# Optimization experiments

Measured on AMD Instinct MI355X. Metric: run time of the kernel, lower is better.

The kernel has to match this reference:

```python
import jax, jax.numpy as jnp
import numpy as np

C = 256
HEADS = 8
HD = C // HEADS
EPS = 1e-5


def _layernorm(x, g, b):
    mu = jnp.mean(x, axis=-1, keepdims=True)
    var = jnp.var(x, axis=-1, keepdims=True)
    return (x - mu) * jax.lax.rsqrt(var + EPS) * g + b


def setup_inputs() -> dict:
    key = jax.random.key(0)
    ks = jax.random.split(key, 16)
    s = 0.02
    return {
        "x": jax.random.normal(ks[0], (1, C, 64, 64), jnp.float32),
        "bn_gamma": 1.0 + s * jax.random.normal(ks[1], (C,), jnp.float32),
        "bn_beta": s * jax.random.normal(ks[2], (C,), jnp.float32),
        "bn_mean": s * jax.random.normal(ks[3], (C,), jnp.float32),
        "bn_var": jnp.ones((C,), jnp.float32),
        "w_in": s * jax.random.normal(ks[4], (C, C), jnp.float32),
        "b_in": jnp.zeros((C,), jnp.float32),
        "ln1_g": jnp.ones((C,), jnp.float32),
        "ln1_b": jnp.zeros((C,), jnp.float32),
        "w_qkv": s * jax.random.normal(ks[5], (3 * C, C), jnp.float32),
        "b_qkv": jnp.zeros((3 * C,), jnp.float32),
        "w_ap": s * jax.random.normal(ks[6], (C, C), jnp.float32),
        "b_ap": jnp.zeros((C,), jnp.float32),
        "ln2_g": jnp.ones((C,), jnp.float32),
        "ln2_b": jnp.zeros((C,), jnp.float32),
        "w_ff1": s * jax.random.normal(ks[7], (4 * C, C), jnp.float32),
        "b_ff1": jnp.zeros((4 * C,), jnp.float32),
        "w_ff2": s * jax.random.normal(ks[8], (C, 4 * C), jnp.float32),
        "b_ff2": jnp.zeros((C,), jnp.float32),
        "w_out": s * jax.random.normal(ks[9], (C, C), jnp.float32),
        "b_out": jnp.zeros((C,), jnp.float32),
    }


def reference(x, bn_gamma, bn_beta, bn_mean, bn_var, w_in, b_in,
              ln1_g, ln1_b, w_qkv, b_qkv, w_ap, b_ap,
              ln2_g, ln2_b, w_ff1, b_ff1, w_ff2, b_ff2, w_out, b_out):
    b, c, h, w = x.shape
    t = h * w
    x_in = x
    # BatchNorm2d (eval mode: running stats)
    xn = (x - bn_mean[None, :, None, None]) * jax.lax.rsqrt(bn_var + EPS)[None, :, None, None]
    xn = xn * bn_gamma[None, :, None, None] + bn_beta[None, :, None, None]
    # proj_in 1x1 conv -> tokens [b, t, c]
    tok = xn.reshape(b, c, t).transpose(0, 2, 1)
    tok = tok @ w_in.T + b_in
    # transformer block (depth=1)
    y = _layernorm(tok, ln1_g, ln1_b)  # norm1
    qkv = y @ w_qkv.T + b_qkv  # [b, t, 3c], channel split (3, H, hd)
    qkv = qkv.reshape(b, t, 3, HEADS, HD)
    q = qkv[:, :, 0].transpose(0, 2, 1, 3)  # [b, H, t, hd]
    k = qkv[:, :, 1].transpose(0, 2, 1, 3)
    v = qkv[:, :, 2].transpose(0, 2, 1, 3)
    scale = HD ** (-0.5)
    attn = jax.nn.softmax(jnp.einsum('bhqd,bhkd->bhqk', q, k) * scale, axis=-1)
    o = jnp.einsum('bhqk,bhkd->bhqd', attn, v)  # [b, H, t, hd]
    o = o.transpose(0, 2, 1, 3).reshape(b, t, c)  # channels ordered (H, hd)
    o = o @ w_ap.T + b_ap  # attn proj 1x1
    attn_out = o + y  # VanillaAttention residual adds its (normed) input
    tok = tok + attn_out
    # FFN
    z = _layernorm(tok, ln2_g, ln2_b)
    z = jax.nn.gelu(z @ w_ff1.T + b_ff1, approximate=False)
    tok = tok + (z @ w_ff2.T + b_ff2)
    # back to image, proj_out 1x1, outer residual
    x4 = tok.transpose(0, 2, 1).reshape(b, c, h, w)
    out = jnp.einsum('oc,bchw->bohw', w_out, x4) + b_out[None, :, None, None]
    return out + x_in
```

## Files before the change

kernel.cpp:

```cpp
#include <hip/hip_runtime.h>
#include <math.h>

#define T_TOK 4096
#define C_DIM 256
#define EPSF  1e-5f
#define SC_QL (0.17677669529663687f * 1.4426950408889634f)

typedef short  bf16x8  __attribute__((ext_vector_type(8)));
typedef float  f32x4   __attribute__((ext_vector_type(4)));
typedef ushort ushort8 __attribute__((ext_vector_type(8)));

__device__ __forceinline__ short f2bf(float f) {
    unsigned u = __builtin_bit_cast(unsigned, f);
    unsigned r = (u + 0x7FFFu + ((u >> 16) & 1u)) >> 16;
    return (short)r;
}
__device__ __forceinline__ float bf2f(ushort u) {
    return __builtin_bit_cast(float, ((unsigned)u) << 16);
}
__device__ __forceinline__ unsigned pk_bf16(float a, float b) {
    const unsigned ua = __builtin_bit_cast(unsigned, a) + 0x8000u;
    const unsigned ub = __builtin_bit_cast(unsigned, b) + 0x8000u;
    return __builtin_amdgcn_perm(ub, ua, 0x07060302u);
}
template <int CTRL>
__device__ __forceinline__ float dppf(float x) {
    return __builtin_bit_cast(float,
        __builtin_amdgcn_mov_dpp(__builtin_bit_cast(int, x), CTRL, 0xF, 0xF, true));
}
__device__ __forceinline__ float rowsum16(float x) {
    x += dppf<0xB1>(x);
    x += dppf<0x4E>(x);
    x += dppf<0x141>(x);
    x += dppf<0x140>(x);
    return x;
}
#define MFMA16(a, b, c) __builtin_amdgcn_mfma_f32_16x16x32_bf16(a, b, c, 0, 0, 0)

__global__ __launch_bounds__(256) void prep_kernel(
    const float* __restrict__ w_in, const float* __restrict__ w_qkv,
    const float* __restrict__ w_ap, const float* __restrict__ w_ff1,
    const float* __restrict__ w_ff2, const float* __restrict__ w_out,
    const float* __restrict__ b_qkv, const float* __restrict__ b_ff1,
    const float* __restrict__ ln1_g, const float* __restrict__ ln1_b,
    const float* __restrict__ ln2_g, const float* __restrict__ ln2_b,
    ushort* __restrict__ wbuf, float* __restrict__ u_all, float* __restrict__ d_all,
    const float* __restrict__ x, const float* __restrict__ gamma,
    const float* __restrict__ beta, const float* __restrict__ mean,
    const float* __restrict__ var, ushort* __restrict__ tin)
{
    __shared__ float tile[32][33];
    if (blockIdx.x < 896) {
        const int gid = blockIdx.x * 256 + threadIdx.x;
        const int e0 = gid * 4;
        const float* src; int off;
        float4 sc = {1.f, 1.f, 1.f, 1.f};
        if (e0 < 65536)       { src = w_in;  off = e0; }
        else if (e0 < 262144) {
            src = w_qkv; off = e0 - 65536;
            const int k = off & 255;
            sc = *(const float4*)(ln1_g + k);
            if (off < 65536) { sc.x *= SC_QL; sc.y *= SC_QL; sc.z *= SC_QL; sc.w *= SC_QL; }
        }
        else if (e0 < 327680) { src = w_ap;  off = e0 - 262144; }
        else if (e0 < 589824) {
            src = w_ff1; off = e0 - 327680;
            sc = *(const float4*)(ln2_g + (off & 255));
        }
        else if (e0 < 851968) { src = w_ff2; off = e0 - 589824; }
        else                  { src = w_out; off = e0 - 851968; }
        const float4 v = *(const float4*)(src + off);
        ushort4 o;
        o.x = (ushort)f2bf(v.x * sc.x); o.y = (ushort)f2bf(v.y * sc.y);
        o.z = (ushort)f2bf(v.z * sc.z); o.w = (ushort)f2bf(v.w * sc.w);
        *(ushort4*)(wbuf + e0) = o;
    } else if (blockIdx.x < 1920) {
        const int bidx = blockIdx.x - 896;
        const int t0 = (bidx & 127) * 32, c0 = (bidx >> 7) * 32;
        const int tx = threadIdx.x & 31, ty = threadIdx.x >> 5;
#pragma unroll
        for (int i = 0; i < 32; i += 8) {
            const int c = c0 + ty + i;
            const float a = rsqrtf(var[c] + EPSF) * gamma[c];
            const float d = beta[c] - mean[c] * a;
            tile[ty + i][tx] = x[c * T_TOK + t0 + tx] * a + d;
        }
        __syncthreads();
#pragma unroll
        for (int i = 0; i < 32; i += 8) {
            const int t = t0 + ty + i;
            tin[t * C_DIM + c0 + tx] = (ushort)f2bf(tile[tx][ty + i]);
        }
    } else {
        const int row = (blockIdx.x - 1920) * 4 + (threadIdx.x >> 6);
        const int lane = threadIdx.x & 63;
        const float* W; const float* gv; const float* bv; float bias; float qs = 1.f;
        if (row < 768) {
            W = w_qkv + (size_t)row * 256; gv = ln1_g; bv = ln1_b; bias = b_qkv[row];
            if (row < 256) qs = SC_QL;
        } else {
            const int r2 = row - 768;
            W = w_ff1 + (size_t)r2 * 256; gv = ln2_g; bv = ln2_b; bias = b_ff1[r2];
        }
        const float4 w4 = *(const float4*)(W + lane * 4);
        const float4 g4 = *(const float4*)(gv + lane * 4);
        const float4 b4 = *(const float4*)(bv + lane * 4);
        float su = w4.x * g4.x + w4.y * g4.y + w4.z * g4.z + w4.w * g4.w;
        float sd = w4.x * b4.x + w4.y * b4.y + w4.z * b4.z + w4.w * b4.w;
#pragma unroll
        for (int off = 32; off > 0; off >>= 1) {
            su += __shfl_xor(su, off);
            sd += __shfl_xor(sd, off);
        }
        if (lane == 0) {
            u_all[row] = qs * su;
            d_all[row] = qs * (sd + bias);
        }
    }
}

__global__ __launch_bounds__(1024) void fused_pre(
    const ushort* __restrict__ tin, const ushort* __restrict__ wb_in,
    const float* __restrict__ b_in, const ushort* __restrict__ wb_qkv,
    const float* __restrict__ u_all, const float* __restrict__ d_all,
    float* __restrict__ tok0, float* __restrict__ lnstats,
    ushort* __restrict__ qkvb)
{
    __shared__ ushort Atile[16 * 264];
    __shared__ ushort Vt[16 * 264];
    __shared__ float  red[16][16][2];
    const int t0 = blockIdx.x * 16;
    const int tid = threadIdx.x, wv = tid >> 6, lane = tid & 63;
    const int c = lane & 15, g = lane >> 4;

    bf16x8 w1[8];
#pragma unroll
    for (int kc = 0; kc < 8; ++kc)
        w1[kc] = *(const bf16x8*)(wb_in + (size_t)(wv * 16 + c) * 256 + kc * 32 + g * 8);

    {
        const int r = tid >> 6, c0 = (tid & 63) * 4;
        *(ushort4*)&Atile[r * 264 + c0] = *(const ushort4*)(tin + (size_t)(t0 + r) * 256 + c0);
    }
    __syncthreads();

    f32x4 acc1 = {};
#pragma unroll
    for (int kc = 0; kc < 8; ++kc) {
        const bf16x8 af = *(const bf16x8*)&Atile[c * 264 + kc * 32 + g * 8];
        acc1 = MFMA16(af, w1[kc], acc1);
    }
    const int colp = wv * 16 + c;
    float vs[4];
    {
        const float bb = b_in[colp];
        float s1[4], s2[4];
#pragma unroll
        for (int rr = 0; rr < 4; ++rr) {
            const float v = acc1[rr] + bb;
            vs[rr] = v; s1[rr] = v; s2[rr] = v * v;
            tok0[(size_t)(t0 + 4 * g + rr) * 256 + colp] = v;
            Vt[(4 * g + rr) * 264 + colp] = (ushort)f2bf(v);
        }
#pragma unroll
        for (int rr = 0; rr < 4; ++rr) { s1[rr] = rowsum16(s1[rr]); s2[rr] = rowsum16(s2[rr]); }
        if (c == 0) {
#pragma unroll
            for (int rr = 0; rr < 4; ++rr) {
                red[wv][4 * g + rr][0] = s1[rr];
                red[wv][4 * g + rr][1] = s2[rr];
            }
        }
    }
    __syncthreads();

    if (tid < 32) {
        const int row = tid >> 1, j = tid & 1;
        float s = 0.f;
#pragma unroll
        for (int w = 0; w < 16; ++w) s += red[w][row][j];
        red[0][row][j] = s;
    }

    f32x4 acc2[3] = {};
#pragma unroll
    for (int kc = 0; kc < 8; ++kc) {
        const bf16x8 af = *(const bf16x8*)&Vt[c * 264 + kc * 32 + g * 8];
#pragma unroll
        for (int nf = 0; nf < 3; ++nf) {
            const bf16x8 bfv = *(const bf16x8*)(wb_qkv +
                (size_t)(wv * 48 + nf * 16 + c) * 256 + kc * 32 + g * 8);
            acc2[nf] = MFMA16(af, bfv, acc2[nf]);
        }
    }
    __syncthreads();

    float mu[4], rs[4];
#pragma unroll
    for (int rr = 0; rr < 4; ++rr) {
        const int row = 4 * g + rr;
        mu[rr] = red[0][row][0] * (1.0f / 256.0f);
        const float var = red[0][row][1] * (1.0f / 256.0f) - mu[rr] * mu[rr];
        rs[rr] = rsqrtf(var + EPSF);
    }
    if (wv == 0 && c == 0) {
#pragma unroll
        for (int rr = 0; rr < 4; ++rr) {
            lnstats[(size_t)(t0 + 4 * g + rr) * 2 + 0] = mu[rr];
            lnstats[(size_t)(t0 + 4 * g + rr) * 2 + 1] = rs[rr];
        }
    }
#pragma unroll
    for (int nf = 0; nf < 3; ++nf) {
        const int col = wv * 48 + nf * 16 + c;
        const float u = u_all[col], d = d_all[col];
#pragma unroll
        for (int rr = 0; rr < 4; ++rr) {
            const float q = rs[rr] * (acc2[nf][rr] - mu[rr] * u) + d;
            qkvb[(size_t)(t0 + 4 * g + rr) * 768 + col] = (ushort)f2bf(q);
        }
    }
}

#define KS   40
#define VTS  72
#define PS_W 34

__global__ __launch_bounds__(256) void attn_mfma(
    const ushort* __restrict__ qkv, ushort* __restrict__ opart,
    float* __restrict__ lpart)
{
    const int h    = blockIdx.y;
    const int q0   = blockIdx.x << 6;
    const int half = blockIdx.z;
    const int tid  = threadIdx.x;
    const int wv   = tid >> 6, lane = tid & 63;
    const int c    = lane & 15, g = lane >> 4;

    __shared__ ushort Ks[2][64 * KS];
    __shared__ ushort Vt[2][32 * VTS];
    __shared__ float  Ps[4][16 * PS_W];

    const bf16x8 qf = *(const bf16x8*)(qkv + (size_t)(q0 + wv * 16 + c) * 768 + h * 32 + g * 8);

    bf16x8 ones;
#pragma unroll
    for (int i = 0; i < 8; ++i) ones[i] = (short)0x3F80;

    f32x4 oacc0 = {0.f, 0.f, 0.f, 0.f};
    f32x4 oacc1 = {0.f, 0.f, 0.f, 0.f};
    f32x4 oaccl = {0.f, 0.f, 0.f, 0.f};

    const int kr = tid >> 2, kc = (tid & 3) * 8;
    const int vp = tid & 31, vd = (tid >> 5) * 4;
    const ushort* kbase = qkv + 256 + h * 32;
    const ushort* vbase = qkv + 512 + h * 32;

    const int kt0 = half * 16, kt1 = kt0 + 16;
    ushort8 kpre  = *(const ushort8*)(kbase + ((size_t)kt0 * 64 + kr) * 768 + kc);
    ushort4 vpre0 = *(const ushort4*)(vbase + ((size_t)kt0 * 64 + 2 * vp) * 768 + vd);
    ushort4 vpre1 = *(const ushort4*)(vbase + ((size_t)kt0 * 64 + 2 * vp + 1) * 768 + vd);

    int p = 0;
    for (int kt = kt0; kt < kt1; ++kt) {
        *(ushort8*)&Ks[p][kr * KS + kc] = kpre;
        {
            unsigned* vtp = (unsigned*)&Vt[p][0];
            vtp[(vd + 0) * (VTS / 2) + vp] = (unsigned)vpre0.x | ((unsigned)vpre1.x << 16);
            vtp[(vd + 1) * (VTS / 2) + vp] = (unsigned)vpre0.y | ((unsigned)vpre1.y << 16);
            vtp[(vd + 2) * (VTS / 2) + vp] = (unsigned)vpre0.z | ((unsigned)vpre1.z << 16);
            vtp[(vd + 3) * (VTS / 2) + vp] = (unsigned)vpre0.w | ((unsigned)vpre1.w << 16);
        }
        __syncthreads();
        if (kt + 1 < kt1) {
            const size_t t0 = (size_t)(kt + 1) * 64;
            kpre  = *(const ushort8*)(kbase + (t0 + kr) * 768 + kc);
            vpre0 = *(const ushort4*)(vbase + (t0 + 2 * vp) * 768 + vd);
            vpre1 = *(const ushort4*)(vbase + (t0 + 2 * vp + 1) * 768 + vd);
        }

        const ushort* ks = &Ks[p][0];
        const ushort* vt = &Vt[p][0];
        const f32x4 zz = {0.f, 0.f, 0.f, 0.f};
        const bf16x8 k0 = *(const bf16x8*)&ks[(0 * 16 + c) * KS + g * 8];
        const bf16x8 k1 = *(const bf16x8*)&ks[(1 * 16 + c) * KS + g * 8];
        const bf16x8 k2 = *(const bf16x8*)&ks[(2 * 16 + c) * KS + g * 8];
        const bf16x8 k3 = *(const bf16x8*)&ks[(3 * 16 + c) * KS + g * 8];
        const f32x4 s0 = MFMA16(k0, qf, zz);
        const f32x4 s1 = MFMA16(k1, qf, zz);
        const f32x4 s2 = MFMA16(k2, qf, zz);
        const f32x4 s3 = MFMA16(k3, qf, zz);

        float* prow = &Ps[wv][c * PS_W];
        {
            const float e00 = __builtin_amdgcn_exp2f(s0[0]), e01 = __builtin_amdgcn_exp2f(s0[1]);
            const float e02 = __builtin_amdgcn_exp2f(s0[2]), e03 = __builtin_amdgcn_exp2f(s0[3]);
            const float e10 = __builtin_amdgcn_exp2f(s1[0]), e11 = __builtin_amdgcn_exp2f(s1[1]);
            const float e12 = __builtin_amdgcn_exp2f(s1[2]), e13 = __builtin_amdgcn_exp2f(s1[3]);
            const float e20 = __builtin_amdgcn_exp2f(s2[0]), e21 = __builtin_amdgcn_exp2f(s2[1]);
            const float e22 = __builtin_amdgcn_exp2f(s2[2]), e23 = __builtin_amdgcn_exp2f(s2[3]);
            const float e30 = __builtin_amdgcn_exp2f(s3[0]), e31 = __builtin_amdgcn_exp2f(s3[1]);
            const float e32 = __builtin_amdgcn_exp2f(s3[2]), e33 = __builtin_amdgcn_exp2f(s3[3]);
            prow[0 * 8 + 2 * g + 0] = __builtin_bit_cast(float, pk_bf16(e00, e01));
            prow[0 * 8 + 2 * g + 1] = __builtin_bit_cast(float, pk_bf16(e02, e03));
            prow[1 * 8 + 2 * g + 0] = __builtin_bit_cast(float, pk_bf16(e10, e11));
            prow[1 * 8 + 2 * g + 1] = __builtin_bit_cast(float, pk_bf16(e12, e13));
            prow[2 * 8 + 2 * g + 0] = __builtin_bit_cast(float, pk_bf16(e20, e21));
            prow[2 * 8 + 2 * g + 1] = __builtin_bit_cast(float, pk_bf16(e22, e23));
            prow[3 * 8 + 2 * g + 0] = __builtin_bit_cast(float, pk_bf16(e30, e31));
            prow[3 * 8 + 2 * g + 1] = __builtin_bit_cast(float, pk_bf16(e32, e33));
        }
#pragma unroll
        for (int ch = 0; ch < 2; ++ch) {
            const float2 pA = *(const float2*)&prow[ch * 16 + 4 * g];
            const float2 pB = *(const float2*)&prow[ch * 16 + 4 * g + 2];
            unsigned pw[4];
            pw[0] = __builtin_bit_cast(unsigned, pA.x);
            pw[1] = __builtin_bit_cast(unsigned, pA.y);
            pw[2] = __builtin_bit_cast(unsigned, pB.x);
            pw[3] = __builtin_bit_cast(unsigned, pB.y);
            const bf16x8 pf = *(const bf16x8*)pw;
            const bf16x8 v0 = *(const bf16x8*)&vt[(c)      * VTS + ch * 32 + g * 8];
            const bf16x8 v1 = *(const bf16x8*)&vt[(16 + c) * VTS + ch * 32 + g * 8];
            oacc0 = MFMA16(pf, v0, oacc0);
            oacc1 = MFMA16(pf, v1, oacc1);
            oaccl = MFMA16(pf, ones, oaccl);
        }
        p ^= 1;
        __syncthreads();
    }

    {
        ushort* op = opart + (size_t)half * (1u << 20) + (size_t)(q0 + wv * 16) * 256 + h * 32;
#pragma unroll
        for (int rr = 0; rr < 4; ++rr) {
            op[(4 * g + rr) * 256 + c]      = (ushort)f2bf(oacc0[rr]);
            op[(4 * g + rr) * 256 + 16 + c] = (ushort)f2bf(oacc1[rr]);
        }
        if (c == 0) {
#pragma unroll
            for (int rr = 0; rr < 4; ++rr)
                lpart[(size_t)(q0 + wv * 16 + 4 * g + rr) * 32 + half * 8 + h] = oaccl[rr];
        }
    }
}

__global__ __launch_bounds__(1024) void fused_mid(
    const ushort* __restrict__ opart, const float* __restrict__ lpart,
    const ushort* __restrict__ wb_ap, const float* __restrict__ b_ap,
    const float* __restrict__ tok0, const float* __restrict__ lnstats,
    const float* __restrict__ ln1_g, const float* __restrict__ ln1_b,
    const ushort* __restrict__ wb_ff1, const float* __restrict__ u_all,
    const float* __restrict__ d_all, float* __restrict__ tok1,
    ushort* __restrict__ zbuf)
{
    __shared__ ushort Otile[16 * 264];
    __shared__ ushort Vt[16 * 264];
    __shared__ float  red[16][16][2];
    const int t0 = blockIdx.x * 16;
    const int tid = threadIdx.x, wv = tid >> 6, lane = tid & 63;
    const int c = lane & 15, g = lane >> 4;

    bf16x8 w1[8];
#pragma unroll
    for (int kc = 0; kc < 8; ++kc)
        w1[kc] = *(const bf16x8*)(wb_ap + (size_t)(wv * 16 + c) * 256 + kc * 32 + g * 8);

    {
        const int r = tid >> 6, c0 = (tid & 63) * 4;
        const int h = (tid & 63) >> 3;
        const float* lp = lpart + (size_t)(t0 + r) * 32;
        const float inv = 1.0f / (lp[h] + lp[8 + h] + lp[16 + h] + lp[24 + h]);
        const size_t base = (size_t)(t0 + r) * 256 + c0;
        const ushort4 a0 = *(const ushort4*)(opart + base);
        const ushort4 a1 = *(const ushort4*)(opart + (1u << 20) + base);
        const ushort4 a2 = *(const ushort4*)(opart + (2u << 20) + base);
        const ushort4 a3 = *(const ushort4*)(opart + (3u << 20) + base);
        unsigned w[2];
        w[0] = pk_bf16((bf2f(a0.x) + bf2f(a1.x) + bf2f(a2.x) + bf2f(a3.x)) * inv,
                       (bf2f(a0.y) + bf2f(a1.y) + bf2f(a2.y) + bf2f(a3.y)) * inv);
        w[1] = pk_bf16((bf2f(a0.z) + bf2f(a1.z) + bf2f(a2.z) + bf2f(a3.z)) * inv,
                       (bf2f(a0.w) + bf2f(a1.w) + bf2f(a2.w) + bf2f(a3.w)) * inv);
        *(ushort4*)&Otile[r * 264 + c0] = *(ushort4*)w;
    }
    __syncthreads();

    f32x4 acc1 = {};
#pragma unroll
    for (int kc = 0; kc < 8; ++kc) {
        const bf16x8 af = *(const bf16x8*)&Otile[c * 264 + kc * 32 + g * 8];
        acc1 = MFMA16(af, w1[kc], acc1);
    }
    const int colp = wv * 16 + c;
    {
        const float bb = b_ap[colp];
        const float g1 = ln1_g[colp], b1 = ln1_b[colp];
        float s1[4], s2[4];
#pragma unroll
        for (int rr = 0; rr < 4; ++rr) {
            const int row = t0 + 4 * g + rr;
            const size_t idx = (size_t)row * 256 + colp;
            const float t0v = tok0[idx];
            const float mu1 = lnstats[(size_t)row * 2 + 0];
            const float rs1 = lnstats[(size_t)row * 2 + 1];
            const float y = (t0v - mu1) * rs1 * g1 + b1;
            const float v = acc1[rr] + bb + y + t0v;
            s1[rr] = v; s2[rr] = v * v;
            tok1[idx] = v;
            Vt[(4 * g + rr) * 264 + colp] = (ushort)f2bf(v);
        }
#pragma unroll
        for (int rr = 0; rr < 4; ++rr) { s1[rr] = rowsum16(s1[rr]); s2[rr] = rowsum16(s2[rr]); }
        if (c == 0) {
#pragma unroll
            for (int rr = 0; rr < 4; ++rr) {
                red[wv][4 * g + rr][0] = s1[rr];
                red[wv][4 * g + rr][1] = s2[rr];
            }
        }
    }
    __syncthreads();

    if (tid < 32) {
        const int row = tid >> 1, j = tid & 1;
        float s = 0.f;
#pragma unroll
        for (int w = 0; w < 16; ++w) s += red[w][row][j];
        red[0][row][j] = s;
    }

    f32x4 acc2[4] = {};
#pragma unroll
    for (int kc = 0; kc < 8; ++kc) {
        const bf16x8 af = *(const bf16x8*)&Vt[c * 264 + kc * 32 + g * 8];
#pragma unroll
        for (int nf = 0; nf < 4; ++nf) {
            const bf16x8 bfv = *(const bf16x8*)(wb_ff1 +
                (size_t)(wv * 64 + nf * 16 + c) * 256 + kc * 32 + g * 8);
            acc2[nf] = MFMA16(af, bfv, acc2[nf]);
        }
    }
    __syncthreads();

    float mu[4], rs[4];
#pragma unroll
    for (int rr = 0; rr < 4; ++rr) {
        const int row = 4 * g + rr;
        mu[rr] = red[0][row][0] * (1.0f / 256.0f);
        const float var = red[0][row][1] * (1.0f / 256.0f) - mu[rr] * mu[rr];
        rs[rr] = rsqrtf(var + EPSF);
    }
#pragma unroll
    for (int nf = 0; nf < 4; ++nf) {
        const int col = wv * 64 + nf * 16 + c;
        const float u = u_all[768 + col], d = d_all[768 + col];
#pragma unroll
        for (int rr = 0; rr < 4; ++rr) {
            float v = rs[rr] * (acc2[nf][rr] - mu[rr] * u) + d;
            v = 0.5f * v * (1.0f + erff(v * 0.70710678118654752f));
            zbuf[(size_t)(t0 + 4 * g + rr) * 1024 + col] = (ushort)f2bf(v);
        }
    }
}

__global__ __launch_bounds__(1024) void fused_post(
    const ushort* __restrict__ zbuf, const ushort* __restrict__ wb_ff2,
    const float* __restrict__ b_ff2, const float* __restrict__ tok1,
    const ushort* __restrict__ wb_out, const float* __restrict__ b_out,
    const float* __restrict__ x, float* __restrict__ out)
{
    __shared__ ushort Ztile[16 * 1032];
    __shared__ ushort T2tile[16 * 264];
    const int t0 = blockIdx.x * 16;
    const int tid = threadIdx.x, wv = tid >> 6, lane = tid & 63;
    const int c = lane & 15, g = lane >> 4;

    bf16x8 w2[8];
#pragma unroll
    for (int kc = 0; kc < 8; ++kc)
        w2[kc] = *(const bf16x8*)(wb_ff2 + (size_t)(wv * 16 + c) * 1024 + kc * 32 + g * 8);

    {
        const int r = tid >> 6, c0 = (tid & 63) * 16;
        *(ushort8*)&Ztile[r * 1032 + c0] =
            *(const ushort8*)(zbuf + (size_t)(t0 + r) * 1024 + c0);
        *(ushort8*)&Ztile[r * 1032 + c0 + 8] =
            *(const ushort8*)(zbuf + (size_t)(t0 + r) * 1024 + c0 + 8);
    }
    __syncthreads();

    f32x4 accf = {};
#pragma unroll
    for (int kc = 0; kc < 8; ++kc) {
        const bf16x8 af = *(const bf16x8*)&Ztile[c * 1032 + kc * 32 + g * 8];
        accf = MFMA16(af, w2[kc], accf);
    }
#pragma unroll
    for (int kc = 8; kc < 32; ++kc) {
        const bf16x8 af = *(const bf16x8*)&Ztile[c * 1032 + kc * 32 + g * 8];
        const bf16x8 bfv = *(const bf16x8*)(wb_ff2 +
            (size_t)(wv * 16 + c) * 1024 + kc * 32 + g * 8);
        accf = MFMA16(af, bfv, accf);
    }
    {
        const int col = wv * 16 + c;
        const float bb = b_ff2[col];
#pragma unroll
        for (int rr = 0; rr < 4; ++rr) {
            const size_t idx = (size_t)(t0 + 4 * g + rr) * 256 + col;
            const float v = accf[rr] + bb + tok1[idx];
            T2tile[(4 * g + rr) * 264 + col] = (ushort)f2bf(v);
        }
    }
    __syncthreads();

    f32x4 acco = {};
#pragma unroll
    for (int kc = 0; kc < 8; ++kc) {
        const bf16x8 bfr = *(const bf16x8*)&T2tile[c * 264 + kc * 32 + g * 8];
        const bf16x8 afr = *(const bf16x8*)(wb_out +
            (size_t)(wv * 16 + c) * 256 + kc * 32 + g * 8);
        acco = MFMA16(afr, bfr, acco);
    }
#pragma unroll
    for (int rr = 0; rr < 4; ++rr) {
        const int och = wv * 16 + 4 * g + rr;
        const size_t idx = (size_t)och * T_TOK + t0 + c;
        out[idx] = acco[rr] + b_out[och] + x[idx];
    }
}

extern "C" void kernel_launch(void* const* d_in, const int* in_sizes, int n_in,
                              void* d_out, int out_size, void* d_ws, size_t ws_size,
                              hipStream_t stream)
{
    const float* x     = (const float*)d_in[0];
    const float* bn_g  = (const float*)d_in[1];
    const float* bn_b  = (const float*)d_in[2];
    const float* bn_m  = (const float*)d_in[3];
    const float* bn_v  = (const float*)d_in[4];
    const float* w_in  = (const float*)d_in[5];
    const float* b_in  = (const float*)d_in[6];
    const float* ln1_g = (const float*)d_in[7];
    const float* ln1_b = (const float*)d_in[8];
    const float* w_qkv = (const float*)d_in[9];
    const float* b_qkv = (const float*)d_in[10];
    const float* w_ap  = (const float*)d_in[11];
    const float* b_ap  = (const float*)d_in[12];
    const float* ln2_g = (const float*)d_in[13];
    const float* ln2_b = (const float*)d_in[14];
    const float* w_ff1 = (const float*)d_in[15];
    const float* b_ff1 = (const float*)d_in[16];
    const float* w_ff2 = (const float*)d_in[17];
    const float* b_ff2 = (const float*)d_in[18];
    const float* w_out = (const float*)d_in[19];
    const float* b_out = (const float*)d_in[20];
    float* out = (float*)d_out;
    float* ws  = (float*)d_ws;

    const size_t MF = 1u << 20;
    float*  tok0   = ws;
    float*  tok1   = ws + MF;
    float*  lnst   = ws + 2 * MF;
    ushort* qkv_bf = (ushort*)(ws + 3 * MF);
    ushort* tin_bf = (ushort*)(ws + 4 * MF + MF / 2);
    ushort* opart  = tin_bf;
    ushort* zbuf   = (ushort*)(ws + 6 * MF + MF / 2);
    float*  lpart  = ws + 8 * MF + MF / 2;
    ushort* wbuf   = (ushort*)(ws + 8 * MF + MF / 2 + 131072);
    const ushort* wb_in  = wbuf;
    const ushort* wb_qkv = wbuf + 65536;
    const ushort* wb_ap  = wbuf + 262144;
    const ushort* wb_ff1 = wbuf + 327680;
    const ushort* wb_ff2 = wbuf + 589824;
    const ushort* wb_out = wbuf + 851968;
    float* u_all = (float*)(wbuf + 917504);
    float* d_all = u_all + 1792;

    prep_kernel<<<2368, 256, 0, stream>>>(
        w_in, w_qkv, w_ap, w_ff1, w_ff2, w_out,
        b_qkv, b_ff1, ln1_g, ln1_b, ln2_g, ln2_b,
        wbuf, u_all, d_all,
        x, bn_g, bn_b, bn_m, bn_v, tin_bf);
    fused_pre<<<256, 1024, 0, stream>>>(tin_bf, wb_in, b_in, wb_qkv,
                                        u_all, d_all, tok0, lnst, qkv_bf);
    attn_mfma<<<dim3(64, 8, 4), 256, 0, stream>>>(qkv_bf, opart, lpart);
    fused_mid<<<256, 1024, 0, stream>>>(opart, lpart, wb_ap, b_ap, tok0, lnst,
                                        ln1_g, ln1_b, wb_ff1, u_all, d_all,
                                        tok1, zbuf);
    fused_post<<<256, 1024, 0, stream>>>(zbuf, wb_ff2, b_ff2, tok1, wb_out, b_out,
                                         x, out);
}
```

Before: 205.0 us.

## Split fused token kernels into quarter-width 256-thread blocks and separate FF2/proj_out

Each 1024-thread fused kernel becomes four 256-thread blocks per 16-token tile, each handling a quarter of the output columns of the second GEMM. The first GEMM (proj_in or attn proj) and its LayerNorm statistics are recomputed redundantly in every quarter block. The post kernel is split into an FF2 kernel writing a bf16 tok2 buffer and a separate proj_out kernel. The aim is more, smaller blocks for better occupancy and scheduling, at the cost of redundant compute, an extra launch and extra global traffic through tok2.

After: 239.7 us. 16.9% more time.

```diff
diff --git a/kernel.cpp b/kernel.cpp
--- a/kernel.cpp
+++ b/kernel.cpp
@@ -58,8 +58,7 @@
         if (e0 < 65536)       { src = w_in;  off = e0; }
         else if (e0 < 262144) {
             src = w_qkv; off = e0 - 65536;
-            const int k = off & 255;
-            sc = *(const float4*)(ln1_g + k);
+            sc = *(const float4*)(ln1_g + (off & 255));
             if (off < 65536) { sc.x *= SC_QL; sc.y *= SC_QL; sc.z *= SC_QL; sc.w *= SC_QL; }
         }
         else if (e0 < 327680) { src = w_ap;  off = e0 - 262144; }
@@ -119,7 +118,7 @@
     }
 }
 
-__global__ __launch_bounds__(1024) void fused_pre(
+__global__ __launch_bounds__(256) void fused_pre(
     const ushort* __restrict__ tin, const ushort* __restrict__ wb_in,
     const float* __restrict__ b_in, const ushort* __restrict__ wb_qkv,
     const float* __restrict__ u_all, const float* __restrict__ d_all,
@@ -128,69 +127,68 @@
 {
     __shared__ ushort Atile[16 * 264];
     __shared__ ushort Vt[16 * 264];
-    __shared__ float  red[16][16][2];
-    const int t0 = blockIdx.x * 16;
+    __shared__ float  red[4][16][2];
+    const int quarter = blockIdx.x & 3;
+    const int t0 = (blockIdx.x >> 2) * 16;
     const int tid = threadIdx.x, wv = tid >> 6, lane = tid & 63;
     const int c = lane & 15, g = lane >> 4;
 
-    bf16x8 w1[8];
-#pragma unroll
-    for (int kc = 0; kc < 8; ++kc)
-        w1[kc] = *(const bf16x8*)(wb_in + (size_t)(wv * 16 + c) * 256 + kc * 32 + g * 8);
-
     {
-        const int r = tid >> 6, c0 = (tid & 63) * 4;
-        *(ushort4*)&Atile[r * 264 + c0] = *(const ushort4*)(tin + (size_t)(t0 + r) * 256 + c0);
-    }
-    __syncthreads();
-
-    f32x4 acc1 = {};
+        const int r = tid >> 4, c0 = (tid & 15) * 16;
+        *(ushort8*)&Atile[r * 264 + c0]     = *(const ushort8*)(tin + (size_t)(t0 + r) * 256 + c0);
+        *(ushort8*)&Atile[r * 264 + c0 + 8] = *(const ushort8*)(tin + (size_t)(t0 + r) * 256 + c0 + 8);
+    }
+    __syncthreads();
+
+    f32x4 a1[4] = {};
 #pragma unroll
     for (int kc = 0; kc < 8; ++kc) {
         const bf16x8 af = *(const bf16x8*)&Atile[c * 264 + kc * 32 + g * 8];
-        acc1 = MFMA16(af, w1[kc], acc1);
-    }
-    const int colp = wv * 16 + c;
-    float vs[4];
-    {
-        const float bb = b_in[colp];
-        float s1[4], s2[4];
-#pragma unroll
-        for (int rr = 0; rr < 4; ++rr) {
-            const float v = acc1[rr] + bb;
-            vs[rr] = v; s1[rr] = v; s2[rr] = v * v;
-            tok0[(size_t)(t0 + 4 * g + rr) * 256 + colp] = v;
-            Vt[(4 * g + rr) * 264 + colp] = (ushort)f2bf(v);
-        }
-#pragma unroll
-        for (int rr = 0; rr < 4; ++rr) { s1[rr] = rowsum16(s1[rr]); s2[rr] = rowsum16(s2[rr]); }
-        if (c == 0) {
-#pragma unroll
-            for (int rr = 0; rr < 4; ++rr) {
-                red[wv][4 * g + rr][0] = s1[rr];
-                red[wv][4 * g + rr][1] = s2[rr];
-            }
+#pragma unroll
+        for (int nf = 0; nf < 4; ++nf) {
+            const bf16x8 bfv = *(const bf16x8*)(wb_in +
+                (size_t)(wv * 64 + nf * 16 + c) * 256 + kc * 32 + g * 8);
+            a1[nf] = MFMA16(af, bfv, a1[nf]);
+        }
+    }
+    float s1[4] = {}, s2[4] = {};
+#pragma unroll
+    for (int nf = 0; nf < 4; ++nf) {
+        const int col = wv * 64 + nf * 16 + c;
+        const float bb = b_in[col];
+#pragma unroll
+        for (int rr = 0; rr < 4; ++rr) {
+            const float v = a1[nf][rr] + bb;
+            s1[rr] += v; s2[rr] += v * v;
+            Vt[(4 * g + rr) * 264 + col] = (ushort)f2bf(v);
+            if (quarter == 0) tok0[(size_t)(t0 + 4 * g + rr) * 256 + col] = v;
+        }
+    }
+#pragma unroll
+    for (int rr = 0; rr < 4; ++rr) { s1[rr] = rowsum16(s1[rr]); s2[rr] = rowsum16(s2[rr]); }
+    if (c == 0) {
+#pragma unroll
+        for (int rr = 0; rr < 4; ++rr) {
+            red[wv][4 * g + rr][0] = s1[rr];
+            red[wv][4 * g + rr][1] = s2[rr];
         }
     }
     __syncthreads();
 
     if (tid < 32) {
         const int row = tid >> 1, j = tid & 1;
-        float s = 0.f;
-#pragma unroll
-        for (int w = 0; w < 16; ++w) s += red[w][row][j];
-        red[0][row][j] = s;
-    }
-
-    f32x4 acc2[3] = {};
+        red[0][row][j] = red[0][row][j] + red[1][row][j] + red[2][row][j] + red[3][row][j];
+    }
+
+    f32x4 a2[3] = {};
 #pragma unroll
     for (int kc = 0; kc < 8; ++kc) {
         const bf16x8 af = *(const bf16x8*)&Vt[c * 264 + kc * 32 + g * 8];
 #pragma unroll
         for (int nf = 0; nf < 3; ++nf) {
             const bf16x8 bfv = *(const bf16x8*)(wb_qkv +
-                (size_t)(wv * 48 + nf * 16 + c) * 256 + kc * 32 + g * 8);
-            acc2[nf] = MFMA16(af, bfv, acc2[nf]);
+                (size_t)(quarter * 192 + wv * 48 + nf * 16 + c) * 256 + kc * 32 + g * 8);
+            a2[nf] = MFMA16(af, bfv, a2[nf]);
         }
     }
     __syncthreads();
@@ -203,7 +201,7 @@
         const float var = red[0][row][1] * (1.0f / 256.0f) - mu[rr] * mu[rr];
         rs[rr] = rsqrtf(var + EPSF);
     }
-    if (wv == 0 && c == 0) {
+    if (quarter == 0 && wv == 0 && c == 0) {
 #pragma unroll
         for (int rr = 0; rr < 4; ++rr) {
             lnstats[(size_t)(t0 + 4 * g + rr) * 2 + 0] = mu[rr];
@@ -212,11 +210,11 @@
     }
 #pragma unroll
     for (int nf = 0; nf < 3; ++nf) {
-        const int col = wv * 48 + nf * 16 + c;
+        const int col = quarter * 192 + wv * 48 + nf * 16 + c;
         const float u = u_all[col], d = d_all[col];
 #pragma unroll
         for (int rr = 0; rr < 4; ++rr) {
-            const float q = rs[rr] * (acc2[nf][rr] - mu[rr] * u) + d;
+            const float q = rs[rr] * (a2[nf][rr] - mu[rr] * u) + d;
             qkvb[(size_t)(t0 + 4 * g + rr) * 768 + col] = (ushort)f2bf(q);
         }
     }
@@ -345,7 +343,7 @@
     }
 }
 
-__global__ __launch_bounds__(1024) void fused_mid(
+__global__ __launch_bounds__(256) void fused_mid(
     const ushort* __restrict__ opart, const float* __restrict__ lpart,
     const ushort* __restrict__ wb_ap, const float* __restrict__ b_ap,
     const float* __restrict__ tok0, const float* __restrict__ lnstats,
@@ -356,88 +354,94 @@
 {
     __shared__ ushort Otile[16 * 264];
     __shared__ ushort Vt[16 * 264];
-    __shared__ float  red[16][16][2];
-    const int t0 = blockIdx.x * 16;
+    __shared__ float  red[4][16][2];
+    const int quarter = blockIdx.x & 3;
+    const int t0 = (blockIdx.x >> 2) * 16;
     const int tid = threadIdx.x, wv = tid >> 6, lane = tid & 63;
     const int c = lane & 15, g = lane >> 4;
 
-    bf16x8 w1[8];
-#pragma unroll
-    for (int kc = 0; kc < 8; ++kc)
-        w1[kc] = *(const bf16x8*)(wb_ap + (size_t)(wv * 16 + c) * 256 + kc * 32 + g * 8);
-
     {
-        const int r = tid >> 6, c0 = (tid & 63) * 4;
-        const int h = (tid & 63) >> 3;
+        const int r = tid >> 4, c0 = (tid & 15) * 16;
+        const int h = c0 >> 5;
         const float* lp = lpart + (size_t)(t0 + r) * 32;
         const float inv = 1.0f / (lp[h] + lp[8 + h] + lp[16 + h] + lp[24 + h]);
         const size_t base = (size_t)(t0 + r) * 256 + c0;
-        const ushort4 a0 = *(const ushort4*)(opart + base);
-        const ushort4 a1 = *(const ushort4*)(opart + (1u << 20) + base);
-        const ushort4 a2 = *(const ushort4*)(opart + (2u << 20) + base);
-        const ushort4 a3 = *(const ushort4*)(opart + (3u << 20) + base);
-        unsigned w[2];
-        w[0] = pk_bf16((bf2f(a0.x) + bf2f(a1.x) + bf2f(a2.x) + bf2f(a3.x)) * inv,
-                       (bf2f(a0.y) + bf2f(a1.y) + bf2f(a2.y) + bf2f(a3.y)) * inv);
-        w[1] = pk_bf16((bf2f(a0.z) + bf2f(a1.z) + bf2f(a2.z) + bf2f(a3.z)) * inv,
-                       (bf2f(a0.w) + bf2f(a1.w) + bf2f(a2.w) + bf2f(a3.w)) * inv);
-        *(ushort4*)&Otile[r * 264 + c0] = *(ushort4*)w;
-    }
-    __syncthreads();
-
-    f32x4 acc1 = {};
+#pragma unroll
+        for (int cc = 0; cc < 16; cc += 4) {
+            const ushort4 a0 = *(const ushort4*)(opart + base + cc);
+            const ushort4 a1 = *(const ushort4*)(opart + (1u << 20) + base + cc);
+            const ushort4 a2 = *(const ushort4*)(opart + (2u << 20) + base + cc);
+            const ushort4 a3 = *(const ushort4*)(opart + (3u << 20) + base + cc);
+            unsigned w[2];
+            w[0] = pk_bf16((bf2f(a0.x) + bf2f(a1.x) + bf2f(a2.x) + bf2f(a3.x)) * inv,
+                           (bf2f(a0.y) + bf2f(a1.y) + bf2f(a2.y) + bf2f(a3.y)) * inv);
+            w[1] = pk_bf16((bf2f(a0.z) + bf2f(a1.z) + bf2f(a2.z) + bf2f(a3.z)) * inv,
+                           (bf2f(a0.w) + bf2f(a1.w) + bf2f(a2.w) + bf2f(a3.w)) * inv);
+            *(ushort4*)&Otile[r * 264 + c0 + cc] = *(ushort4*)w;
+        }
+    }
+    __syncthreads();
+
+    f32x4 a1[4] = {};
 #pragma unroll
     for (int kc = 0; kc < 8; ++kc) {
         const bf16x8 af = *(const bf16x8*)&Otile[c * 264 + kc * 32 + g * 8];
-        acc1 = MFMA16(af, w1[kc], acc1);
-    }
-    const int colp = wv * 16 + c;
-    {
-        const float bb = b_ap[colp];
-        const float g1 = ln1_g[colp], b1 = ln1_b[colp];
-        float s1[4], s2[4];
-#pragma unroll
-        for (int rr = 0; rr < 4; ++rr) {
-            const int row = t0 + 4 * g + rr;
-            const size_t idx = (size_t)row * 256 + colp;
+#pragma unroll
+        for (int nf = 0; nf < 4; ++nf) {
+            const bf16x8 bfv = *(const bf16x8*)(wb_ap +
+                (size_t)(wv * 64 + nf * 16 + c) * 256 + kc * 32 + g * 8);
+            a1[nf] = MFMA16(af, bfv, a1[nf]);
+        }
+    }
+    float mu1[4], rs1[4];
+#pragma unroll
+    for (int rr = 0; rr < 4; ++rr) {
+        const int row = t0 + 4 * g + rr;
+        mu1[rr] = lnstats[(size_t)row * 2 + 0];
+        rs1[rr] = lnstats[(size_t)row * 2 + 1];
+    }
+    float s1[4] = {}, s2[4] = {};
+#pragma unroll
+    for (int nf = 0; nf < 4; ++nf) {
+        const int col = wv * 64 + nf * 16 + c;
+        const float bb = b_ap[col];
+        const float g1 = ln1_g[col], b1 = ln1_b[col];
+#pragma unroll
+        for (int rr = 0; rr < 4; ++rr) {
+            const size_t idx = (size_t)(t0 + 4 * g + rr) * 256 + col;
             const float t0v = tok0[idx];
-            const float mu1 = lnstats[(size_t)row * 2 + 0];
-            const float rs1 = lnstats[(size_t)row * 2 + 1];
-            const float y = (t0v - mu1) * rs1 * g1 + b1;
-            const float v = acc1[rr] + bb + y + t0v;
-            s1[rr] = v; s2[rr] = v * v;
-            tok1[idx] = v;
-            Vt[(4 * g + rr) * 264 + colp] = (ushort)f2bf(v);
-        }
-#pragma unroll
-        for (int rr = 0; rr < 4; ++rr) { s1[rr] = rowsum16(s1[rr]); s2[rr] = rowsum16(s2[rr]); }
-        if (c == 0) {
-#pragma unroll
-            for (int rr = 0; rr < 4; ++rr) {
-                red[wv][4 * g + rr][0] = s1[rr];
-                red[wv][4 * g + rr][1] = s2[rr];
-            }
+            const float y = (t0v - mu1[rr]) * rs1[rr] * g1 + b1;
+            const float v = a1[nf][rr] + bb + y + t0v;
+            s1[rr] += v; s2[rr] += v * v;
+            Vt[(4 * g + rr) * 264 + col] = (ushort)f2bf(v);
+            if (quarter == 0) tok1[idx] = v;
+        }
+    }
+#pragma unroll
+    for (int rr = 0; rr < 4; ++rr) { s1[rr] = rowsum16(s1[rr]); s2[rr] = rowsum16(s2[rr]); }
+    if (c == 0) {
+#pragma unroll
+        for (int rr = 0; rr < 4; ++rr) {
+            red[wv][4 * g + rr][0] = s1[rr];
+            red[wv][4 * g + rr][1] = s2[rr];
         }
     }
     __syncthreads();
 
     if (tid < 32) {
         const int row = tid >> 1, j = tid & 1;
-        float s = 0.f;
-#pragma unroll
-        for (int w = 0; w < 16; ++w) s += red[w][row][j];
-        red[0][row][j] = s;
-    }
-
-    f32x4 acc2[4] = {};
+        red[0][row][j] = red[0][row][j] + red[1][row][j] + red[2][row][j] + red[3][row][j];
+    }
+
+    f32x4 a2[4] = {};
 #pragma unroll
     for (int kc = 0; kc < 8; ++kc) {
         const bf16x8 af = *(const bf16x8*)&Vt[c * 264 + kc * 32 + g * 8];
 #pragma unroll
         for (int nf = 0; nf < 4; ++nf) {
             const bf16x8 bfv = *(const bf16x8*)(wb_ff1 +
-                (size_t)(wv * 64 + nf * 16 + c) * 256 + kc * 32 + g * 8);
-            acc2[nf] = MFMA16(af, bfv, acc2[nf]);
+                (size_t)(quarter * 256 + wv * 64 + nf * 16 + c) * 256 + kc * 32 + g * 8);
+            a2[nf] = MFMA16(af, bfv, a2[nf]);
         }
     }
     __syncthreads();
@@ -452,81 +456,98 @@
     }
 #pragma unroll
     for (int nf = 0; nf < 4; ++nf) {
-        const int col = wv * 64 + nf * 16 + c;
+        const int col = quarter * 256 + wv * 64 + nf * 16 + c;
         const float u = u_all[768 + col], d = d_all[768 + col];
 #pragma unroll
         for (int rr = 0; rr < 4; ++rr) {
-            float v = rs[rr] * (acc2[nf][rr] - mu[rr] * u) + d;
+            float v = rs[rr] * (a2[nf][rr] - mu[rr] * u) + d;
             v = 0.5f * v * (1.0f + erff(v * 0.70710678118654752f));
             zbuf[(size_t)(t0 + 4 * g + rr) * 1024 + col] = (ushort)f2bf(v);
         }
     }
 }
 
-__global__ __launch_bounds__(1024) void fused_post(
+__global__ __launch_bounds__(256) void k_ff2(
     const ushort* __restrict__ zbuf, const ushort* __restrict__ wb_ff2,
     const float* __restrict__ b_ff2, const float* __restrict__ tok1,
-    const ushort* __restrict__ wb_out, const float* __restrict__ b_out,
-    const float* __restrict__ x, float* __restrict__ out)
+    ushort* __restrict__ tok2)
 {
     __shared__ ushort Ztile[16 * 1032];
-    __shared__ ushort T2tile[16 * 264];
-    const int t0 = blockIdx.x * 16;
+    const int quarter = blockIdx.x & 3;
+    const int t0 = (blockIdx.x >> 2) * 16;
     const int tid = threadIdx.x, wv = tid >> 6, lane = tid & 63;
     const int c = lane & 15, g = lane >> 4;
 
+    const int col = quarter * 64 + wv * 16 + c;
     bf16x8 w2[8];
 #pragma unroll
     for (int kc = 0; kc < 8; ++kc)
-        w2[kc] = *(const bf16x8*)(wb_ff2 + (size_t)(wv * 16 + c) * 1024 + kc * 32 + g * 8);
+        w2[kc] = *(const bf16x8*)(wb_ff2 + (size_t)col * 1024 + kc * 32 + g * 8);
 
     {
-        const int r = tid >> 6, c0 = (tid & 63) * 16;
-        *(ushort8*)&Ztile[r * 1032 + c0] =
-            *(const ushort8*)(zbuf + (size_t)(t0 + r) * 1024 + c0);
-        *(ushort8*)&Ztile[r * 1032 + c0 + 8] =
-            *(const ushort8*)(zbuf + (size_t)(t0 + r) * 1024 + c0 + 8);
-    }
-    __syncthreads();
-
-    f32x4 accf = {};
+        const int r = tid >> 4, c0 = (tid & 15) * 64;
+#pragma unroll
+        for (int i = 0; i < 8; ++i)
+            *(ushort8*)&Ztile[r * 1032 + c0 + i * 8] =
+                *(const ushort8*)(zbuf + (size_t)(t0 + r) * 1024 + c0 + i * 8);
+    }
+    __syncthreads();
+
+    f32x4 acc = {};
 #pragma unroll
     for (int kc = 0; kc < 8; ++kc) {
         const bf16x8 af = *(const bf16x8*)&Ztile[c * 1032 + kc * 32 + g * 8];
-        accf = MFMA16(af, w2[kc], accf);
+        acc = MFMA16(af, w2[kc], acc);
     }
 #pragma unroll
     for (int kc = 8; kc < 32; ++kc) {
         const bf16x8 af = *(const bf16x8*)&Ztile[c * 1032 + kc * 32 + g * 8];
-        const bf16x8 bfv = *(const bf16x8*)(wb_ff2 +
-            (size_t)(wv * 16 + c) * 1024 + kc * 32 + g * 8);
-        accf = MFMA16(af, bfv, accf);
-    }
+        const bf16x8 bfv = *(const bf16x8*)(wb_ff2 + (size_t)col * 1024 + kc * 32 + g * 8);
+        acc = MFMA16(af, bfv, acc);
+    }
+    const float bb = b_ff2[col];
+#pragma unroll
+    for (int rr = 0; rr < 4; ++rr) {
+        const size_t idx = (size_t)(t0 + 4 * g + rr) * 256 + col;
+        tok2[idx] = (ushort)f2bf(acc[rr] + bb + tok1[idx]);
+    }
+}
+
+__global__ __launch_bounds__(256) void k_pout(
+    const ushort* __restrict__ tok2, const ushort* __restrict__ wb_out,
+    const float* __restrict__ b_out, const float* __restrict__ x,
+    float* __restrict__ out)
+{
+    __shared__ ushort Ttile[16 * 264];
+    const int quarter = blockIdx.x & 3;
+    const int t0 = (blockIdx.x >> 2) * 16;
+    const int tid = threadIdx.x, wv = tid >> 6, lane = tid & 63;
+    const int c = lane & 15, g = lane >> 4;
+
+    bf16x8 wo[8];
+#pragma unroll
+    for (int kc = 0; kc < 8; ++kc)
+        wo[kc] = *(const bf16x8*)(wb_out +
+            (size_t)(quarter * 64 + wv * 16 + c) * 256 + kc * 32 + g * 8);
+
     {
-        const int col = wv * 16 + c;
-        const float bb = b_ff2[col];
-#pragma unroll
-        for (int rr = 0; rr < 4; ++rr) {
-            const size_t idx = (size_t)(t0 + 4 * g + rr) * 256 + col;
-            const float v = accf[rr] + bb + tok1[idx];
-            T2tile[(4 * g + rr) * 264 + col] = (ushort)f2bf(v);
-        }
-    }
-    __syncthreads();
-
-    f32x4 acco = {};
+        const int r = tid >> 4, c0 = (tid & 15) * 16;
+        *(ushort8*)&Ttile[r * 264 + c0]     = *(const ushort8*)(tok2 + (size_t)(t0 + r) * 256 + c0);
+        *(ushort8*)&Ttile[r * 264 + c0 + 8] = *(const ushort8*)(tok2 + (size_t)(t0 + r) * 256 + c0 + 8);
+    }
+    __syncthreads();
+
+    f32x4 acc = {};
 #pragma unroll
     for (int kc = 0; kc < 8; ++kc) {
-        const bf16x8 bfr = *(const bf16x8*)&T2tile[c * 264 + kc * 32 + g * 8];
-        const bf16x8 afr = *(const bf16x8*)(wb_out +
-            (size_t)(wv * 16 + c) * 256 + kc * 32 + g * 8);
-        acco = MFMA16(afr, bfr, acco);
+        const bf16x8 bfr = *(const bf16x8*)&Ttile[c * 264 + kc * 32 + g * 8];
+        acc = MFMA16(wo[kc], bfr, acc);
     }
 #pragma unroll
     for (int rr = 0; rr < 4; ++rr) {
-        const int och = wv * 16 + 4 * g + rr;
+        const int och = quarter * 64 + wv * 16 + 4 * g + rr;
         const size_t idx = (size_t)och * T_TOK + t0 + c;
-        out[idx] = acco[rr] + b_out[och] + x[idx];
+        out[idx] = acc[rr] + b_out[och] + x[idx];
     }
 }
 
@@ -562,6 +583,7 @@
     float*  tok0   = ws;
     float*  tok1   = ws + MF;
     float*  lnst   = ws + 2 * MF;
+    ushort* tok2   = (ushort*)(ws + 2 * MF + MF / 4);
     ushort* qkv_bf = (ushort*)(ws + 3 * MF);
     ushort* tin_bf = (ushort*)(ws + 4 * MF + MF / 2);
     ushort* opart  = tin_bf;
@@ -582,12 +604,12 @@
         b_qkv, b_ff1, ln1_g, ln1_b, ln2_g, ln2_b,
         wbuf, u_all, d_all,
         x, bn_g, bn_b, bn_m, bn_v, tin_bf);
-    fused_pre<<<256, 1024, 0, stream>>>(tin_bf, wb_in, b_in, wb_qkv,
+    fused_pre<<<1024, 256, 0, stream>>>(tin_bf, wb_in, b_in, wb_qkv,
                                         u_all, d_all, tok0, lnst, qkv_bf);
     attn_mfma<<<dim3(64, 8, 4), 256, 0, stream>>>(qkv_bf, opart, lpart);
-    fused_mid<<<256, 1024, 0, stream>>>(opart, lpart, wb_ap, b_ap, tok0, lnst,
+    fused_mid<<<1024, 256, 0, stream>>>(opart, lpart, wb_ap, b_ap, tok0, lnst,
                                         ln1_g, ln1_b, wb_ff1, u_all, d_all,
                                         tok1, zbuf);
-    fused_post<<<256, 1024, 0, stream>>>(zbuf, wb_ff2, b_ff2, tok1, wb_out, b_out,
-                                         x, out);
-}
+    k_ff2<<<1024, 256, 0, stream>>>(zbuf, wb_ff2, b_ff2, tok1, tok2);
+    k_pout<<<1024, 256, 0, stream>>>(tok2, wb_out, b_out, x, out);
+}
```
